# Kernel optimization log

Measured on AMD Instinct MI355X. Metric: run time of the kernel, lower is better.

Reference implementation:

```python
import jax, jax.numpy as jnp
import numpy as np

D = 1024   # d_model
HS = 64    # head_size
H = D // HS
B, T = 4, 2048
EPS = 1e-5


def setup_inputs() -> dict:
    key = jax.random.key(0)
    ks = jax.random.split(key, 8)
    s = 1.0 / np.sqrt(D)
    mk = lambda k: (jax.random.normal(k, (D, D), jnp.float32) * s)
    return {
        "x": jax.random.normal(ks[0], (B, T, D), jnp.float32),
        "ln_g": jnp.ones((D,), jnp.float32),
        "ln_b": jnp.zeros((D,), jnp.float32),
        "Wx": mk(ks[1]),
        "Ww": mk(ks[2]),
        "bw": jnp.zeros((D,), jnp.float32),
        "Wk": mk(ks[3]),
        "Wv": mk(ks[4]),
        "Wr": mk(ks[5]),
        "Wo": mk(ks[6]),
    }


def reference(x, ln_g, ln_b, Wx, Ww, bw, Wk, Wv, Wr, Wo):
    Bb, Tt, C = x.shape
    nh, hs = C // HS, HS
    # LayerNorm (population variance, matching torch nn.LayerNorm)
    mu = x.mean(-1, keepdims=True)
    var = x.var(-1, keepdims=True)
    xn = (x - mu) / jnp.sqrt(var + EPS) * ln_g + ln_b
    # projections (weights stored pre-transposed: y = x @ W)
    w = jax.nn.sigmoid((xn @ Wx) @ Ww + bw).reshape(Bb, Tt, nh, hs)
    k = (xn @ Wk).reshape(Bb, Tt, nh, hs)
    v = (xn @ Wv).reshape(Bb, Tt, nh, hs)
    r = jax.nn.sigmoid(xn @ Wr).reshape(Bb, Tt, nh, hs)

    def step(state, inp):
        kt, vt, wt, rt = inp  # each [B, H, hs]
        # outer product kv [B,H,hs,hs]; row-wise decay by (1 - w_t)
        state = (1.0 - wt)[..., None] * state + kt[..., None] * vt[..., None, :]
        out = jnp.einsum('bhd,bhde->bhe', rt, state)
        return state, out

    init = jnp.zeros((Bb, nh, hs, hs), x.dtype)
    tm = lambda a: jnp.moveaxis(a, 1, 0)  # time-major for scan
    state, outs = jax.lax.scan(step, init, (tm(k), tm(v), tm(w), tm(r)))
    y = jnp.moveaxis(outs, 0, 1).reshape(Bb, Tt, C) @ Wo
    return (y, state)
```

## Files before the change

kernel.cpp:

```cpp
#include <hip/hip_runtime.h>

#define ROWS 8192
#define DD   1024
#define TT   2048
#define NH   16
#define HS   64
#define CH   64
#define NC   (TT / CH)

typedef __attribute__((ext_vector_type(8))) short short8;
typedef __attribute__((ext_vector_type(4))) float f32x4;
typedef __attribute__((ext_vector_type(4))) unsigned short us4;
typedef unsigned short u16;

__device__ __forceinline__ u16 f2bf(float f) {
  unsigned u = __builtin_bit_cast(unsigned, f);
  u += 0x7fffu + ((u >> 16) & 1u);
  return (u16)(u >> 16);
}

__device__ __forceinline__ void gload16(const void* g, void* l) {
  __builtin_amdgcn_global_load_lds(
      (const __attribute__((address_space(1))) unsigned int*)g,
      (__attribute__((address_space(3))) unsigned int*)l, 16, 0, 0);
}

__global__ __launch_bounds__(256) void transpose_cast(const float* __restrict__ W,
                                                      u16* __restrict__ WT) {
  __shared__ float tile[32][33];
  const int tx = threadIdx.x, ty = threadIdx.y;
  const int bx = blockIdx.x, by = blockIdx.y;
#pragma unroll
  for (int j = 0; j < 4; ++j)
    tile[ty + j * 8][tx] = W[(size_t)(by * 32 + ty + j * 8) * DD + bx * 32 + tx];
  __syncthreads();
#pragma unroll
  for (int j = 0; j < 4; ++j)
    WT[(size_t)(bx * 32 + ty + j * 8) * DD + by * 32 + tx] = f2bf(tile[tx][ty + j * 8]);
}

__global__ __launch_bounds__(256) void ln_kernel(const float* __restrict__ x,
                                                 const float* __restrict__ g,
                                                 const float* __restrict__ b,
                                                 u16* __restrict__ xn) {
  const int row = blockIdx.x;
  const int tid = threadIdx.x;
  const float4 v = reinterpret_cast<const float4*>(x + (size_t)row * DD)[tid];
  float s = v.x + v.y + v.z + v.w;
  float s2 = v.x * v.x + v.y * v.y + v.z * v.z + v.w * v.w;
#pragma unroll
  for (int o = 32; o > 0; o >>= 1) { s += __shfl_down(s, o); s2 += __shfl_down(s2, o); }
  __shared__ float red[8];
  const int wv = tid >> 6;
  if ((tid & 63) == 0) { red[wv] = s; red[4 + wv] = s2; }
  __syncthreads();
  s = red[0] + red[1] + red[2] + red[3];
  s2 = red[4] + red[5] + red[6] + red[7];
  const float mu = s * (1.f / 1024.f);
  const float var = s2 * (1.f / 1024.f) - mu * mu;
  const float rstd = rsqrtf(var + 1e-5f);
  const float4 gg = reinterpret_cast<const float4*>(g)[tid];
  const float4 bb = reinterpret_cast<const float4*>(b)[tid];
  us4 o4;
  o4.x = f2bf((v.x - mu) * rstd * gg.x + bb.x);
  o4.y = f2bf((v.y - mu) * rstd * gg.y + bb.y);
  o4.z = f2bf((v.z - mu) * rstd * gg.z + bb.z);
  o4.w = f2bf((v.w - mu) * rstd * gg.w + bb.w);
  *reinterpret_cast<us4*>(xn + (size_t)row * DD + tid * 4) = o4;
}

template <int EPI>
__global__ __launch_bounds__(256) void gemm_bt(const u16* __restrict__ A,
                                               const u16* __restrict__ BT,
                                               float* __restrict__ Cf,
                                               u16* __restrict__ Cb,
                                               const float* __restrict__ bias,
                                               int M, int N, int K) {
  __shared__ u16 lA[2][128 * 32];
  __shared__ u16 lB[2][128 * 32];
  const int tid = threadIdx.x;
  const int bx = blockIdx.x, by = blockIdx.y;
  const int lane = tid & 63, wid = tid >> 6;
  const int wr = wid >> 1, wc = wid & 1;
  const int sr = tid >> 2, sc = (tid & 3) * 8;
  const u16* gA = A + (size_t)(by * 128 + sr) * K + sc;
  const u16* gB = BT + (size_t)(bx * 128 + sr) * K + sc;

  f32x4 acc[4][4];
#pragma unroll
  for (int m = 0; m < 4; ++m)
#pragma unroll
    for (int n = 0; n < 4; ++n) acc[m][n] = (f32x4){0.f, 0.f, 0.f, 0.f};

  auto stage = [&](int buf, int kt) {
    const u16* a0 = gA + kt * 32;
    const u16* b0 = gB + kt * 32;
    gload16(a0, &lA[buf][tid * 8]);
    gload16(a0 + (size_t)64 * K, &lA[buf][2048 + tid * 8]);
    gload16(b0, &lB[buf][tid * 8]);
    gload16(b0 + (size_t)64 * K, &lB[buf][2048 + tid * 8]);
  };

  stage(0, 0);
  const int fr = lane & 15, fk = (lane >> 4) * 8;
  int cur = 0;
  const int nk = K / 32;
  for (int kt = 0; kt < nk; ++kt) {
    __syncthreads();
    if (kt + 1 < nk) stage(cur ^ 1, kt + 1);
    short8 af[4], bv[4];
#pragma unroll
    for (int m = 0; m < 4; ++m)
      af[m] = *reinterpret_cast<const short8*>(&lA[cur][(wr * 64 + m * 16 + fr) * 32 + fk]);
#pragma unroll
    for (int n = 0; n < 4; ++n)
      bv[n] = *reinterpret_cast<const short8*>(&lB[cur][(wc * 64 + n * 16 + fr) * 32 + fk]);
#pragma unroll
    for (int m = 0; m < 4; ++m)
#pragma unroll
      for (int n = 0; n < 4; ++n)
        acc[m][n] = __builtin_amdgcn_mfma_f32_16x16x32_bf16(af[m], bv[n], acc[m][n], 0, 0, 0);
    cur ^= 1;
  }

  const int er = (lane >> 4) * 4, ec = lane & 15;
#pragma unroll
  for (int m = 0; m < 4; ++m) {
    const int row0 = by * 128 + wr * 64 + m * 16 + er;
#pragma unroll
    for (int n = 0; n < 4; ++n) {
      const int col = bx * 128 + wc * 64 + n * 16 + ec;
#pragma unroll
      for (int i = 0; i < 4; ++i) {
        const float val = acc[m][n][i];
        const size_t idx = (size_t)(row0 + i) * N + col;
        if constexpr (EPI == 0) {
          Cb[idx] = f2bf(val);
        } else if constexpr (EPI == 1) {
          Cf[idx] = val;
        } else if constexpr (EPI == 2) {
          Cf[idx] = 1.f / (1.f + __expf(-val));
        } else {
          const float z = val + bias[col];
          Cf[idx] = 1.f / (1.f + __expf(z));
        }
      }
    }
  }
}

__global__ __launch_bounds__(256) void scan_phase1(const float* __restrict__ omw,
                                                   const float* __restrict__ kk,
                                                   const float* __restrict__ vv,
                                                   float* __restrict__ U,
                                                   float* __restrict__ P) {
  const int c = blockIdx.x, bh = blockIdx.y;
  const int tid = threadIdx.x;
  const int lane = tid & 63;
  const int dbase = __builtin_amdgcn_readfirstlane((tid >> 6) << 4);
  const size_t chainBase = (size_t)(bh >> 4) * TT * DD + (size_t)(bh & 15) * HS;
  size_t base = chainBase + (size_t)c * CH * DD;

  float st[16];
#pragma unroll
  for (int i = 0; i < 16; ++i) st[i] = 0.f;
  const int pd = dbase + (lane & 15);
  float vp = 1.f;

  float ve = vv[base + lane];
  for (int t = 0; t < CH; ++t) {
    const float* __restrict__ op = omw + base;
    const float* __restrict__ kp = kk + base;
    const size_t nbase = (t + 1 < CH) ? (base + DD) : base;
    const float ve_n = vv[nbase + lane];
    vp *= op[pd];
#pragma unroll
    for (int i = 0; i < 16; ++i)
      st[i] = __builtin_fmaf(op[dbase + i], st[i], kp[dbase + i] * ve);
    ve = ve_n;
    base += DD;
  }
  float* __restrict__ Ub = U + ((size_t)c * 64 + bh) * 4096;
#pragma unroll
  for (int i = 0; i < 16; ++i) Ub[(dbase + i) * 64 + lane] = st[i];
  if (lane < 16) P[((size_t)c * 64 + bh) * 64 + dbase + lane] = vp;
}

__global__ __launch_bounds__(256) void scan_phase2(float* __restrict__ U,
                                                   const float* __restrict__ P,
                                                   float* __restrict__ stateOut) {
  const int bh = blockIdx.x;
  const int ds = blockIdx.y;
  const int tid = threadIdx.x;
  const int d = ds * 4 + (tid >> 6);
  const int e = tid & 63;
  const size_t el = (size_t)d * 64 + e;

  float S = 0.f;
  size_t ub = (size_t)bh * 4096 + el;
  size_t pb = (size_t)bh * 64 + d;
  for (int c = 0; c < NC; ++c) {
    const float u_c = U[ub];
    const float p_c = P[pb];
    U[ub] = S;
    S = __builtin_fmaf(p_c, S, u_c);
    ub += (size_t)64 * 4096;
    pb += (size_t)64 * 64;
  }
  stateOut[(size_t)bh * 4096 + el] = S;
}

__global__ __launch_bounds__(256) void scan_phase3(const float* __restrict__ omw,
                                                   const float* __restrict__ kk,
                                                   const float* __restrict__ vv,
                                                   const float* __restrict__ rr,
                                                   const float* __restrict__ S_start,
                                                   u16* __restrict__ outs) {
  __shared__ float part[2][4][64];
  const int c = blockIdx.x, bh = blockIdx.y;
  const int tid = threadIdx.x;
  const int lane = tid & 63;
  const int wid = tid >> 6;
  const int dbase = __builtin_amdgcn_readfirstlane(wid << 4);
  const size_t chainBase = (size_t)(bh >> 4) * TT * DD + (size_t)(bh & 15) * HS;
  size_t base = chainBase + (size_t)c * CH * DD;

  float st[16];
  const float* __restrict__ Sb = S_start + ((size_t)c * 64 + bh) * 4096;
#pragma unroll
  for (int i = 0; i < 16; ++i) st[i] = Sb[(dbase + i) * 64 + lane];

  float ve = vv[base + lane];
  for (int t = 0; t < CH; ++t) {
    const float* __restrict__ op = omw + base;
    const float* __restrict__ kp = kk + base;
    const float* __restrict__ rp = rr + base;
    const size_t nbase = (t + 1 < CH) ? (base + DD) : base;
    const float ve_n = vv[nbase + lane];

    float a0 = 0.f, a1 = 0.f, a2 = 0.f, a3 = 0.f;
#pragma unroll
    for (int i = 0; i < 4; ++i) {
      st[i] = __builtin_fmaf(op[dbase + i], st[i], kp[dbase + i] * ve);
      a0 = __builtin_fmaf(rp[dbase + i], st[i], a0);
      st[4 + i] = __builtin_fmaf(op[dbase + 4 + i], st[4 + i], kp[dbase + 4 + i] * ve);
      a1 = __builtin_fmaf(rp[dbase + 4 + i], st[4 + i], a1);
      st[8 + i] = __builtin_fmaf(op[dbase + 8 + i], st[8 + i], kp[dbase + 8 + i] * ve);
      a2 = __builtin_fmaf(rp[dbase + 8 + i], st[8 + i], a2);
      st[12 + i] = __builtin_fmaf(op[dbase + 12 + i], st[12 + i], kp[dbase + 12 + i] * ve);
      a3 = __builtin_fmaf(rp[dbase + 12 + i], st[12 + i], a3);
    }
    part[t & 1][wid][lane] = (a0 + a1) + (a2 + a3);
    __syncthreads();
    if (wid == 0) {
      const float s = (part[t & 1][0][lane] + part[t & 1][1][lane]) +
                      (part[t & 1][2][lane] + part[t & 1][3][lane]);
      outs[base + lane] = f2bf(s);
    }
    ve = ve_n;
    base += DD;
  }
}

extern "C" void kernel_launch(void* const* d_in, const int* in_sizes, int n_in,
                              void* d_out, int out_size, void* d_ws, size_t ws_size,
                              hipStream_t stream) {
  const float* x   = (const float*)d_in[0];
  const float* lng = (const float*)d_in[1];
  const float* lnb = (const float*)d_in[2];
  const float* Wx  = (const float*)d_in[3];
  const float* Ww  = (const float*)d_in[4];
  const float* bw  = (const float*)d_in[5];
  const float* Wk  = (const float*)d_in[6];
  const float* Wv  = (const float*)d_in[7];
  const float* Wr  = (const float*)d_in[8];
  const float* Wo  = (const float*)d_in[9];
  float* out = (float*)d_out;
  char* ws = (char*)d_ws;

  const size_t SZ_W = (size_t)DD * DD * 2;
  u16* WxT = (u16*)(ws + 0 * SZ_W);
  u16* WwT = (u16*)(ws + 1 * SZ_W);
  u16* WkT = (u16*)(ws + 2 * SZ_W);
  u16* WvT = (u16*)(ws + 3 * SZ_W);
  u16* WrT = (u16*)(ws + 4 * SZ_W);
  u16* WoT = (u16*)(ws + 5 * SZ_W);
  size_t off = 6 * SZ_W;
  const size_t SZ_ABF = (size_t)ROWS * DD * 2;
  u16* xn   = (u16*)(ws + off); off += SZ_ABF;
  u16* pbuf = (u16*)(ws + off); off += SZ_ABF;
  u16* outs = (u16*)(ws + off); off += SZ_ABF;
  const size_t SZ_AF = (size_t)ROWS * DD * 4;
  float* omw = (float*)(ws + off); off += SZ_AF;
  float* kf  = (float*)(ws + off); off += SZ_AF;
  float* vf  = (float*)(ws + off); off += SZ_AF;
  float* rf  = (float*)(ws + off); off += SZ_AF;
  float* Ubuf = (float*)xn;
  float* Pbuf = (float*)WxT;
  (void)ws_size; (void)in_sizes; (void)n_in; (void)out_size;

  dim3 tpb(32, 8), tgrid(32, 32);
  transpose_cast<<<tgrid, tpb, 0, stream>>>(Wx, WxT);
  transpose_cast<<<tgrid, tpb, 0, stream>>>(Ww, WwT);
  transpose_cast<<<tgrid, tpb, 0, stream>>>(Wk, WkT);
  transpose_cast<<<tgrid, tpb, 0, stream>>>(Wv, WvT);
  transpose_cast<<<tgrid, tpb, 0, stream>>>(Wr, WrT);
  transpose_cast<<<tgrid, tpb, 0, stream>>>(Wo, WoT);

  ln_kernel<<<ROWS, 256, 0, stream>>>(x, lng, lnb, xn);

  dim3 ggrid(DD / 128, ROWS / 128), gblk(256);
  gemm_bt<0><<<ggrid, gblk, 0, stream>>>(xn, WxT, nullptr, pbuf, nullptr, ROWS, DD, DD);
  gemm_bt<3><<<ggrid, gblk, 0, stream>>>(pbuf, WwT, omw, nullptr, bw, ROWS, DD, DD);
  gemm_bt<1><<<ggrid, gblk, 0, stream>>>(xn, WkT, kf, nullptr, nullptr, ROWS, DD, DD);
  gemm_bt<1><<<ggrid, gblk, 0, stream>>>(xn, WvT, vf, nullptr, nullptr, ROWS, DD, DD);
  gemm_bt<2><<<ggrid, gblk, 0, stream>>>(xn, WrT, rf, nullptr, nullptr, ROWS, DD, DD);

  dim3 sgrid(NC, 64);
  scan_phase1<<<sgrid, 256, 0, stream>>>(omw, kf, vf, Ubuf, Pbuf);
  dim3 p2grid(64, 16);
  scan_phase2<<<p2grid, 256, 0, stream>>>(Ubuf, Pbuf, out + (size_t)ROWS * DD);
  scan_phase3<<<sgrid, 256, 0, stream>>>(omw, kf, vf, rf, Ubuf, outs);

  gemm_bt<1><<<ggrid, gblk, 0, stream>>>(outs, WoT, out, nullptr, nullptr, ROWS, DD, DD);
}
```

Measured before the change: 515.5 us.

## Halve scan chunk size, store chunk states in bf16, batch phase3 output reduction

Chunk length drops from 64 to 32, which doubles the number of parallel chunks in the scan's phase 1 and phase 3. Per-chunk partial states are stored as bf16 to keep the U buffer the same size and reduce traffic. Phase 2 now prefetches the next chunk's values. Phase 3 buffers 16 timesteps of partial sums in shared memory and reduces them across all waves with two barriers per 16 steps instead of one barrier per step. The cost is lower precision in the chunk-start states and a longer sequential phase 2 chain.

Result: faster. 495.8 us (-3.8%).

```diff
diff --git a/kernel.cpp b/kernel.cpp
--- a/kernel.cpp
+++ b/kernel.cpp
@@ -5,7 +5,7 @@
 #define TT   2048
 #define NH   16
 #define HS   64
-#define CH   64
+#define CH   32
 #define NC   (TT / CH)
 
 typedef __attribute__((ext_vector_type(8))) short short8;
@@ -17,6 +17,10 @@
   unsigned u = __builtin_bit_cast(unsigned, f);
   u += 0x7fffu + ((u >> 16) & 1u);
   return (u16)(u >> 16);
+}
+
+__device__ __forceinline__ float bf2f(u16 h) {
+  return __builtin_bit_cast(float, (unsigned)h << 16);
 }
 
 __device__ __forceinline__ void gload16(const void* g, void* l) {
@@ -152,7 +156,7 @@
 __global__ __launch_bounds__(256) void scan_phase1(const float* __restrict__ omw,
                                                    const float* __restrict__ kk,
                                                    const float* __restrict__ vv,
-                                                   float* __restrict__ U,
+                                                   u16* __restrict__ U,
                                                    float* __restrict__ P) {
   const int c = blockIdx.x, bh = blockIdx.y;
   const int tid = threadIdx.x;
@@ -180,13 +184,13 @@
     ve = ve_n;
     base += DD;
   }
-  float* __restrict__ Ub = U + ((size_t)c * 64 + bh) * 4096;
-#pragma unroll
-  for (int i = 0; i < 16; ++i) Ub[(dbase + i) * 64 + lane] = st[i];
+  u16* __restrict__ Ub = U + ((size_t)c * 64 + bh) * 4096;
+#pragma unroll
+  for (int i = 0; i < 16; ++i) Ub[(dbase + i) * 64 + lane] = f2bf(st[i]);
   if (lane < 16) P[((size_t)c * 64 + bh) * 64 + dbase + lane] = vp;
 }
 
-__global__ __launch_bounds__(256) void scan_phase2(float* __restrict__ U,
+__global__ __launch_bounds__(256) void scan_phase2(u16* __restrict__ U,
                                                    const float* __restrict__ P,
                                                    float* __restrict__ stateOut) {
   const int bh = blockIdx.x;
@@ -199,11 +203,17 @@
   float S = 0.f;
   size_t ub = (size_t)bh * 4096 + el;
   size_t pb = (size_t)bh * 64 + d;
+  u16 u_c = U[ub];
+  float p_c = P[pb];
   for (int c = 0; c < NC; ++c) {
-    const float u_c = U[ub];
-    const float p_c = P[pb];
-    U[ub] = S;
-    S = __builtin_fmaf(p_c, S, u_c);
+    u16 u_n = u_c; float p_n = p_c;
+    if (c + 1 < NC) {
+      u_n = U[ub + (size_t)64 * 4096];
+      p_n = P[pb + (size_t)64 * 64];
+    }
+    U[ub] = f2bf(S);
+    S = __builtin_fmaf(p_c, S, bf2f(u_c));
+    u_c = u_n; p_c = p_n;
     ub += (size_t)64 * 4096;
     pb += (size_t)64 * 64;
   }
@@ -214,51 +224,54 @@
                                                    const float* __restrict__ kk,
                                                    const float* __restrict__ vv,
                                                    const float* __restrict__ rr,
-                                                   const float* __restrict__ S_start,
+                                                   const u16* __restrict__ S_start,
                                                    u16* __restrict__ outs) {
-  __shared__ float part[2][4][64];
+  __shared__ float part[4][16][64];
   const int c = blockIdx.x, bh = blockIdx.y;
   const int tid = threadIdx.x;
   const int lane = tid & 63;
   const int wid = tid >> 6;
   const int dbase = __builtin_amdgcn_readfirstlane(wid << 4);
   const size_t chainBase = (size_t)(bh >> 4) * TT * DD + (size_t)(bh & 15) * HS;
-  size_t base = chainBase + (size_t)c * CH * DD;
+  const size_t base0 = chainBase + (size_t)c * CH * DD;
+  size_t base = base0;
 
   float st[16];
-  const float* __restrict__ Sb = S_start + ((size_t)c * 64 + bh) * 4096;
-#pragma unroll
-  for (int i = 0; i < 16; ++i) st[i] = Sb[(dbase + i) * 64 + lane];
+  const u16* __restrict__ Sb = S_start + ((size_t)c * 64 + bh) * 4096;
+#pragma unroll
+  for (int i = 0; i < 16; ++i) st[i] = bf2f(Sb[(dbase + i) * 64 + lane]);
 
   float ve = vv[base + lane];
-  for (int t = 0; t < CH; ++t) {
-    const float* __restrict__ op = omw + base;
-    const float* __restrict__ kp = kk + base;
-    const float* __restrict__ rp = rr + base;
-    const size_t nbase = (t + 1 < CH) ? (base + DD) : base;
-    const float ve_n = vv[nbase + lane];
-
-    float a0 = 0.f, a1 = 0.f, a2 = 0.f, a3 = 0.f;
-#pragma unroll
-    for (int i = 0; i < 4; ++i) {
-      st[i] = __builtin_fmaf(op[dbase + i], st[i], kp[dbase + i] * ve);
-      a0 = __builtin_fmaf(rp[dbase + i], st[i], a0);
-      st[4 + i] = __builtin_fmaf(op[dbase + 4 + i], st[4 + i], kp[dbase + 4 + i] * ve);
-      a1 = __builtin_fmaf(rp[dbase + 4 + i], st[4 + i], a1);
-      st[8 + i] = __builtin_fmaf(op[dbase + 8 + i], st[8 + i], kp[dbase + 8 + i] * ve);
-      a2 = __builtin_fmaf(rp[dbase + 8 + i], st[8 + i], a2);
-      st[12 + i] = __builtin_fmaf(op[dbase + 12 + i], st[12 + i], kp[dbase + 12 + i] * ve);
-      a3 = __builtin_fmaf(rp[dbase + 12 + i], st[12 + i], a3);
+  for (int w2 = 0; w2 < CH / 16; ++w2) {
+#pragma unroll
+    for (int tt = 0; tt < 16; ++tt) {
+      const float* __restrict__ op = omw + base;
+      const float* __restrict__ kp = kk + base;
+      const float* __restrict__ rp = rr + base;
+      const size_t nbase = (w2 * 16 + tt + 1 < CH) ? (base + DD) : base;
+      const float ve_n = vv[nbase + lane];
+
+      float a0 = 0.f, a1 = 0.f;
+#pragma unroll
+      for (int i = 0; i < 8; ++i) {
+        st[i] = __builtin_fmaf(op[dbase + i], st[i], kp[dbase + i] * ve);
+        a0 = __builtin_fmaf(rp[dbase + i], st[i], a0);
+        st[8 + i] = __builtin_fmaf(op[dbase + 8 + i], st[8 + i], kp[dbase + 8 + i] * ve);
+        a1 = __builtin_fmaf(rp[dbase + 8 + i], st[8 + i], a1);
+      }
+      part[wid][tt][lane] = a0 + a1;
+      ve = ve_n;
+      base += DD;
     }
-    part[t & 1][wid][lane] = (a0 + a1) + (a2 + a3);
     __syncthreads();
-    if (wid == 0) {
-      const float s = (part[t & 1][0][lane] + part[t & 1][1][lane]) +
-                      (part[t & 1][2][lane] + part[t & 1][3][lane]);
-      outs[base + lane] = f2bf(s);
+#pragma unroll
+    for (int s = 0; s < 4; ++s) {
+      const int tt = wid * 4 + s;
+      const float sum = (part[0][tt][lane] + part[1][tt][lane]) +
+                        (part[2][tt][lane] + part[3][tt][lane]);
+      outs[base0 + (size_t)(w2 * 16 + tt) * DD + lane] = f2bf(sum);
     }
-    ve = ve_n;
-    base += DD;
+    __syncthreads();
   }
 }
 
@@ -295,7 +308,7 @@
   float* kf  = (float*)(ws + off); off += SZ_AF;
   float* vf  = (float*)(ws + off); off += SZ_AF;
   float* rf  = (float*)(ws + off); off += SZ_AF;
-  float* Ubuf = (float*)xn;
+  u16*   Ubuf = xn;
   float* Pbuf = (float*)WxT;
   (void)ws_size; (void)in_sizes; (void)n_in; (void)out_size;
 
```
